# Performance work log

Hardware: AMD Instinct MI355X
Metric: run time of the kernel (lower is better)

Reference implementation:

```python
import jax, jax.numpy as jnp
import numpy as np

BN_EPS = 1e-5

def _bn(x, g, b, m, v):
    # eval-mode BatchNorm1d over channel dim of [B, C, N]
    scale = g / jnp.sqrt(v + BN_EPS)
    return (x - m[:, None]) * scale[:, None] + b[:, None]

def _conv1(W, x, b=None):
    # 1x1 Conv1d == channel matmul: W [O, C], x [B, C, N] -> [B, O, N]
    y = jnp.einsum('oc,bcn->bon', W, x)
    if b is not None:
        y = y + b[:, None]
    return y

def _sa_layer(x, wqk, wv, bv, wt, bt, g, b, m, v):
    # offset self-attention; q_conv and k_conv share weights
    xk = _conv1(wqk, x)                          # [B, D, N]
    xq = jnp.swapaxes(xk, 1, 2)                  # [B, N, D]
    xv = _conv1(wv, x, bv)                       # [B, D, N]
    energy = jnp.einsum('bnd,bdm->bnm', xq, xk)  # [B, N, N]
    attn = jax.nn.softmax(energy, axis=-1)
    attn = attn / (1e-9 + attn.sum(axis=1, keepdims=True))  # L1 renorm over dim=1
    x_r = jnp.einsum('bdn,bnm->bdm', xv, attn)   # [B, D, N]
    x_r = jax.nn.relu(_bn(_conv1(wt, x - x_r, bt), g, b, m, v))
    return x + x_r

def setup_inputs() -> dict:
    key = jax.random.key(0)
    ks = iter(jax.random.split(key, 64))
    B, Cin, N = 16, 3, 2048
    D, F, H1, OUT = 128, 1024, 512, 50
    def rn(shape, s=0.05):
        return jax.random.normal(next(ks), shape, dtype=jnp.float32) * s
    def var(shape):
        return jax.random.uniform(next(ks), shape, dtype=jnp.float32) * 0.5 + 0.5
    inp = {
        'x': jax.random.normal(next(ks), (B, Cin, N), dtype=jnp.float32),
        'w1': rn((D, Cin)), 'w2': rn((D, D)),
        'bn1_g': jnp.ones((D,)), 'bn1_b': jnp.zeros((D,)), 'bn1_m': rn((D,)), 'bn1_v': var((D,)),
        'bn2_g': jnp.ones((D,)), 'bn2_b': jnp.zeros((D,)), 'bn2_m': rn((D,)), 'bn2_v': var((D,)),
        'sa_wqk': rn((4, D, D)), 'sa_wv': rn((4, D, D)), 'sa_bv': rn((4, D)),
        'sa_wt': rn((4, D, D)), 'sa_bt': rn((4, D)),
        'sa_g': jnp.ones((4, D)), 'sa_b': jnp.zeros((4, D)), 'sa_m': rn((4, D)), 'sa_v': var((4, D)),
        'wf': rn((F, 4 * D)),
        'bnf_g': jnp.ones((F,)), 'bnf_b': jnp.zeros((F,)), 'bnf_m': rn((F,)), 'bnf_v': var((F,)),
        'ws1': rn((H1, 3 * F)), 'bs1': rn((H1,)),
        'bns1_g': jnp.ones((H1,)), 'bns1_b': jnp.zeros((H1,)), 'bns1_m': rn((H1,)), 'bns1_v': var((H1,)),
        'ws2': rn((OUT, H1)), 'bs2': rn((OUT,)),
        'bns2_g': jnp.ones((OUT,)), 'bns2_b': jnp.zeros((OUT,)), 'bns2_m': rn((OUT,)), 'bns2_v': var((OUT,)),
    }
    return inp

def reference(x, w1, w2, bn1_g, bn1_b, bn1_m, bn1_v, bn2_g, bn2_b, bn2_m, bn2_v,
              sa_wqk, sa_wv, sa_bv, sa_wt, sa_bt, sa_g, sa_b, sa_m, sa_v,
              wf, bnf_g, bnf_b, bnf_m, bnf_v,
              ws1, bs1, bns1_g, bns1_b, bns1_m, bns1_v,
              ws2, bs2, bns2_g, bns2_b, bns2_m, bns2_v):
    B, _, N = x.shape
    h = jax.nn.relu(_bn(_conv1(w1, x), bn1_g, bn1_b, bn1_m, bn1_v))
    h = jax.nn.relu(_bn(_conv1(w2, h), bn2_g, bn2_b, bn2_m, bn2_v))
    feats = []
    for i in range(4):
        h = _sa_layer(h, sa_wqk[i], sa_wv[i], sa_bv[i], sa_wt[i], sa_bt[i],
                      sa_g[i], sa_b[i], sa_m[i], sa_v[i])
        feats.append(h)
    cat = jnp.concatenate(feats, axis=1)                 # [B, 512, N]
    fused = _bn(_conv1(wf, cat), bnf_g, bnf_b, bnf_m, bnf_v)
    fused = jnp.where(fused >= 0, fused, 0.2 * fused)    # LeakyReLU(0.2)
    x_max = fused.max(axis=2)                            # [B, 1024]
    x_avg = fused.mean(axis=2)                           # [B, 1024]
    gmax = jnp.broadcast_to(x_max[:, :, None], (B, x_max.shape[1], N))
    gavg = jnp.broadcast_to(x_avg[:, :, None], (B, x_avg.shape[1], N))
    h = jnp.concatenate([fused, gmax, gavg], axis=1)     # [B, 3072, N]
    h = jax.nn.relu(_bn(_conv1(ws1, h, bs1), bns1_g, bns1_b, bns1_m, bns1_v))
    # dropout is identity in eval mode
    h = jax.nn.relu(_bn(_conv1(ws2, h, bs2), bns2_g, bns2_b, bns2_m, bns2_v))
    return h  # [B, out_channel, N]
```

## Files before the change

### kernel.cpp

```cpp
#include <hip/hip_runtime.h>
#include <cstdint>
#include <cstddef>

#define B_   16
#define N_   2048
#define D_   128
#define F_   1024
#define H1_  512
#define OUT_ 50

static constexpr float BN_EPS = 1e-5f;

typedef __attribute__((ext_vector_type(8))) short short8;
typedef __attribute__((ext_vector_type(4))) float f32x4;

__device__ inline unsigned short f2bf(float f) {
  union { float f; unsigned u; } v; v.f = f;
  unsigned r = v.u + 0x7fff + ((v.u >> 16) & 1);
  return (unsigned short)(r >> 16);
}
__device__ inline float bf2f(unsigned short h) {
  union { unsigned u; float f; } v; v.u = ((unsigned)h) << 16; return v.f;
}

__device__ inline void dma16(const unsigned short* g, unsigned short* l) {
  __builtin_amdgcn_global_load_lds(
      (const __attribute__((address_space(1))) unsigned int*)g,
      (__attribute__((address_space(3))) unsigned int*)l, 16, 0, 0);
}

__global__ void foldw_k(const float* __restrict__ W, int ldW,
                        const float* __restrict__ bias,
                        const float* __restrict__ g, const float* __restrict__ bb,
                        const float* __restrict__ m, const float* __restrict__ v,
                        unsigned short* __restrict__ Wb, float* __restrict__ biasF,
                        int O, int Opad, int K) {
  long i = (long)blockIdx.x * 256 + threadIdx.x;
  if (i >= (long)Opad * K) return;
  int o = (int)(i / K), k = (int)(i % K);
  float sc = 1.f, sh = 0.f;
  if (o < O && g) { sc = g[o] * rsqrtf(v[o] + BN_EPS); sh = bb[o] - m[o] * sc; }
  float w = (o < O) ? W[(long)o * ldW + k] * sc : 0.f;
  Wb[i] = f2bf(w);
  if (k == 0 && biasF) {
    float bf = 0.f;
    if (o < O) bf = (bias ? bias[o] : 0.f) * sc + sh;
    biasF[o] = bf;
  }
}

__global__ void conv1_k(const float* __restrict__ x, const float* __restrict__ w1,
                        const float* __restrict__ g, const float* __restrict__ bb,
                        const float* __restrict__ m, const float* __restrict__ v,
                        unsigned short* __restrict__ h0b) {
  int o = threadIdx.x, n = blockIdx.x, b = blockIdx.y;
  const float* xb = x + (long)b * 3 * N_;
  float val = w1[o * 3 + 0] * xb[n] + w1[o * 3 + 1] * xb[N_ + n] + w1[o * 3 + 2] * xb[2 * N_ + n];
  float sc = g[o] * rsqrtf(v[o] + BN_EPS);
  val = val * sc + (bb[o] - m[o] * sc);
  h0b[((long)b * N_ + n) * D_ + o] = f2bf(fmaxf(val, 0.f));
}

template <int TM>
__global__ __launch_bounds__(256, 4)
void gemm_tok(const unsigned short* __restrict__ Wb, int ldW,
              const unsigned short* __restrict__ A, long sA, int ldA,
              const float* __restrict__ biasF,
              const float* __restrict__ perBO, int ldPBO,
              const unsigned short* __restrict__ resH, long sRes, int ldRes,
              unsigned short* __restrict__ outH, long sOutH, int ldOutH,
              float* __restrict__ pmax, float* __restrict__ psum,
              int K, int act, int flags) {
  constexpr int MT = TM / 32;
  __shared__ unsigned short lAB[TM * 64 + 128 * 64];
  __shared__ float lpm[4][64], lps[4][64];
  unsigned short* lA = lAB;
  unsigned short* lB = lAB + TM * 64;
  unsigned short* lS = lAB;
  int tid = threadIdx.x;
  int n0 = blockIdx.x * TM, o0 = blockIdx.y * 128, b = blockIdx.z;
  int wave = tid >> 6, lane = tid & 63;
  int wr = wave >> 1, wc = wave & 1;
  int quad = lane >> 4, l15 = lane & 15;
  int rowL = lane >> 3;
  int kseg = (lane & 7) ^ rowL;
  const unsigned short* Ab = A + (long)b * sA + (long)n0 * ldA;
  const unsigned short* Wp = Wb + (long)o0 * ldW;

  f32x4 acc[MT][4];
  #pragma unroll
  for (int i = 0; i < MT; ++i)
    #pragma unroll
    for (int j = 0; j < 4; ++j) acc[i][j] = (f32x4){0.f, 0.f, 0.f, 0.f};

  for (int kc = 0; kc < K; kc += 64) {
    #pragma unroll
    for (int t = 0; t < 4; ++t) {
      int chunk = t * 4 + wave;
      dma16(Wp + (long)(chunk * 8 + rowL) * ldW + kc + kseg * 8, &lB[chunk * 512]);
      if (chunk < TM / 8)
        dma16(Ab + (long)(chunk * 8 + rowL) * ldA + kc + kseg * 8, &lA[chunk * 512]);
    }
    __syncthreads();
    #pragma unroll
    for (int kk = 0; kk < 2; ++kk) {
      short8 af[MT], bf[4];
      #pragma unroll
      for (int mt = 0; mt < MT; ++mt) {
        int r = wr * (TM / 2) + mt * 16 + l15;
        af[mt] = *(const short8*)&lA[r * 64 + (((kk * 4 + quad) ^ (l15 & 7)) * 8)];
      }
      #pragma unroll
      for (int ot = 0; ot < 4; ++ot) {
        int r = wc * 64 + ot * 16 + l15;
        bf[ot] = *(const short8*)&lB[r * 64 + (((kk * 4 + quad) ^ (l15 & 7)) * 8)];
      }
      #pragma unroll
      for (int mt = 0; mt < MT; ++mt)
        #pragma unroll
        for (int ot = 0; ot < 4; ++ot)
          acc[mt][ot] = __builtin_amdgcn_mfma_f32_16x16x32_bf16(bf[ot], af[mt], acc[mt][ot], 0, 0, 0);
    }
    __syncthreads();
  }

  bool doPool = (flags & 32) != 0;
  #pragma unroll
  for (int ot = 0; ot < 4; ++ot) {
    int obL = wc * 64 + ot * 16 + quad * 4;
    int ob = o0 + obL;
    float bi[4] = {0.f, 0.f, 0.f, 0.f};
    if (biasF) { float4 t = *(const float4*)&biasF[ob]; bi[0] = t.x; bi[1] = t.y; bi[2] = t.z; bi[3] = t.w; }
    if (perBO) {
      float4 t = *(const float4*)&perBO[(long)b * ldPBO + ob];
      bi[0] += t.x; bi[1] += t.y; bi[2] += t.z; bi[3] += t.w;
    }
    float pm4[4], ps4[4];
    #pragma unroll
    for (int r = 0; r < 4; ++r) { pm4[r] = -1e30f; ps4[r] = 0.f; }
    int g = obL >> 3, go = obL & 7;
    #pragma unroll
    for (int mt = 0; mt < MT; ++mt) {
      int nL = wr * (TM / 2) + mt * 16 + l15;
      float vals[4];
      #pragma unroll
      for (int r = 0; r < 4; ++r) {
        float val = acc[mt][ot][r] + bi[r];
        if (act == 1)      val = fmaxf(val, 0.f);
        else if (act == 2) val = (val >= 0.f) ? val : 0.2f * val;
        vals[r] = val;
      }
      if (flags & 16) {
        uint2 rv = *(const uint2*)&resH[(long)b * sRes + (long)(n0 + nL) * ldRes + ob];
        unsigned short rr[4];
        *(uint2*)rr = rv;
        #pragma unroll
        for (int r = 0; r < 4; ++r) vals[r] += bf2f(rr[r]);
      }
      unsigned short t4[4];
      #pragma unroll
      for (int r = 0; r < 4; ++r) {
        t4[r] = f2bf(vals[r]);
        if (doPool) { pm4[r] = fmaxf(pm4[r], vals[r]); ps4[r] += vals[r]; }
      }
      int gp = (g & 8) | ((g ^ (nL & 7)) & 7);
      *(uint2*)&lS[nL * 128 + gp * 8 + go] = *(uint2*)&t4[0];
    }
    if (doPool) {
      #pragma unroll
      for (int r = 0; r < 4; ++r) {
        float m = pm4[r], s = ps4[r];
        m = fmaxf(m, __shfl_xor(m, 1)); s += __shfl_xor(s, 1);
        m = fmaxf(m, __shfl_xor(m, 2)); s += __shfl_xor(s, 2);
        m = fmaxf(m, __shfl_xor(m, 4)); s += __shfl_xor(s, 4);
        m = fmaxf(m, __shfl_xor(m, 8)); s += __shfl_xor(s, 8);
        if (l15 == 0) { lpm[wave][ot * 16 + quad * 4 + r] = m; lps[wave][ot * 16 + quad * 4 + r] = s; }
      }
    }
  }
  __syncthreads();
  {
    int r0 = tid >> 4, s = tid & 15;
    #pragma unroll
    for (int it = 0; it < TM / 16; ++it) {
      int row = it * 16 + r0;
      int sp = (s & 8) | ((s ^ (row & 7)) & 7);
      short8 v = *(const short8*)&lS[row * 128 + sp * 8];
      *(short8*)&outH[(long)b * sOutH + (long)(n0 + row) * ldOutH + o0 + s * 8] = v;
    }
  }
  if (doPool && tid < 128) {
    int wcx = tid >> 6, ol = tid & 63;
    float m = fmaxf(lpm[wcx][ol], lpm[wcx + 2][ol]);
    float s = lps[wcx][ol] + lps[wcx + 2][ol];
    int o = o0 + wcx * 64 + ol;
    pmax[((long)b * 16 + blockIdx.x) * 1024 + o] = m;
    psum[((long)b * 16 + blockIdx.x) * 1024 + o] = s;
  }
}

template <int TM>
__global__ __launch_bounds__(256, 4)
void gemm_chan(const unsigned short* __restrict__ Wb, int ldW,
               const unsigned short* __restrict__ A, long sA, int ldA,
               const float* __restrict__ biasF,
               float* __restrict__ outF, long sOutF, int ldOutF,
               unsigned short* __restrict__ outH, long sOutH, int ldOutH,
               int K, int O, int act) {
  constexpr int MT = TM / 32;
  __shared__ unsigned short lA[TM * 64];
  __shared__ unsigned short lB[128 * 64];
  int tid = threadIdx.x;
  int n0 = blockIdx.x * TM, o0 = blockIdx.y * 128, b = blockIdx.z;
  int wave = tid >> 6, lane = tid & 63;
  int wr = wave >> 1, wc = wave & 1;
  int quad = lane >> 4, l15 = lane & 15;
  int rowL = lane >> 3;
  int kseg = (lane & 7) ^ rowL;
  const unsigned short* Ab = A + (long)b * sA + (long)n0 * ldA;
  const unsigned short* Wp = Wb + (long)o0 * ldW;

  f32x4 acc[MT][4];
  #pragma unroll
  for (int i = 0; i < MT; ++i)
    #pragma unroll
    for (int j = 0; j < 4; ++j) acc[i][j] = (f32x4){0.f, 0.f, 0.f, 0.f};

  for (int kc = 0; kc < K; kc += 64) {
    #pragma unroll
    for (int t = 0; t < 4; ++t) {
      int chunk = t * 4 + wave;
      dma16(Wp + (long)(chunk * 8 + rowL) * ldW + kc + kseg * 8, &lB[chunk * 512]);
      if (chunk < TM / 8)
        dma16(Ab + (long)(chunk * 8 + rowL) * ldA + kc + kseg * 8, &lA[chunk * 512]);
    }
    __syncthreads();
    #pragma unroll
    for (int kk = 0; kk < 2; ++kk) {
      short8 af[MT], bf[4];
      #pragma unroll
      for (int mt = 0; mt < MT; ++mt) {
        int r = wr * (TM / 2) + mt * 16 + l15;
        af[mt] = *(const short8*)&lA[r * 64 + (((kk * 4 + quad) ^ (l15 & 7)) * 8)];
      }
      #pragma unroll
      for (int ot = 0; ot < 4; ++ot) {
        int r = wc * 64 + ot * 16 + l15;
        bf[ot] = *(const short8*)&lB[r * 64 + (((kk * 4 + quad) ^ (l15 & 7)) * 8)];
      }
      #pragma unroll
      for (int mt = 0; mt < MT; ++mt)
        #pragma unroll
        for (int ot = 0; ot < 4; ++ot)
          acc[mt][ot] = __builtin_amdgcn_mfma_f32_16x16x32_bf16(af[mt], bf[ot], acc[mt][ot], 0, 0, 0);
    }
    __syncthreads();
  }

  #pragma unroll
  for (int ot = 0; ot < 4; ++ot) {
    int o = o0 + wc * 64 + ot * 16 + l15;
    if (o >= O) continue;
    float bi = biasF ? biasF[o] : 0.f;
    #pragma unroll
    for (int mt = 0; mt < MT; ++mt) {
      int nb = n0 + wr * (TM / 2) + mt * 16 + quad * 4;
      float vals[4];
      #pragma unroll
      for (int r = 0; r < 4; ++r) {
        float val = acc[mt][ot][r] + bi;
        if (act == 1)      val = fmaxf(val, 0.f);
        else if (act == 2) val = (val >= 0.f) ? val : 0.2f * val;
        vals[r] = val;
      }
      if (outF)
        *(float4*)&outF[(long)b * sOutF + (long)o * ldOutF + nb] = *(float4*)vals;
      if (outH) {
        unsigned short t[4];
        #pragma unroll
        for (int r = 0; r < 4; ++r) t[r] = f2bf(vals[r]);
        *(uint2*)&outH[(long)b * sOutH + (long)o * ldOutH + nb] = *(uint2*)&t[0];
      }
    }
  }
}

__global__ __launch_bounds__(256)
void gram_lw(const unsigned short* __restrict__ xk, long sXk,
             float* __restrict__ pm, float* __restrict__ ps) {
  __shared__ unsigned short lK[2][64 * 128];
  int tid = threadIdx.x, wave = tid >> 6, lane = tid & 63;
  int quad = lane >> 4, l15 = lane & 15;
  int rowL4 = lane >> 4, s16 = lane & 15;
  int n0 = blockIdx.y * 128, b = blockIdx.x, seg = blockIdx.z;
  int mbase = seg * 1024;
  const unsigned short* Kp = xk + (long)b * sXk;
  short8 afr[2][4];
  #pragma unroll
  for (int g2 = 0; g2 < 2; ++g2) {
    const unsigned short* arow = Kp + (long)(n0 + g2 * 64 + wave * 16 + l15) * 128;
    #pragma unroll
    for (int kf = 0; kf < 4; ++kf) afr[g2][kf] = *(const short8*)(arow + kf * 32 + quad * 8);
  }
  float runm[2][4], runs[2][4];
  #pragma unroll
  for (int g2 = 0; g2 < 2; ++g2)
    #pragma unroll
    for (int r = 0; r < 4; ++r) { runm[g2][r] = -1e30f; runs[g2][r] = 0.f; }

  auto stage = [&](int ch, int bf) {
    #pragma unroll
    for (int t = 0; t < 4; ++t) {
      int c = t * 4 + wave;
      int row = c * 4 + rowL4;
      int gseg = (s16 & 8) | ((s16 ^ (row & 7)) & 7);
      dma16(Kp + (long)(mbase + ch * 64 + row) * 128 + gseg * 8, &lK[bf][c * 512]);
    }
  };
  stage(0, 0);

  for (int ch = 0; ch < 16; ++ch) {
    __syncthreads();
    int bf = ch & 1;
    if (ch + 1 < 16) stage(ch + 1, bf ^ 1);
    f32x4 sv[2][4];
    #pragma unroll
    for (int mf = 0; mf < 4; ++mf) {
      f32x4 sa = (f32x4){0.f, 0.f, 0.f, 0.f};
      f32x4 sb = (f32x4){0.f, 0.f, 0.f, 0.f};
      #pragma unroll
      for (int kf = 0; kf < 4; ++kf) {
        int r = mf * 16 + l15, q = kf * 4 + quad;
        int sp = (q & 8) | ((q ^ (r & 7)) & 7);
        short8 bfr = *(const short8*)&lK[bf][r * 128 + sp * 8];
        sa = __builtin_amdgcn_mfma_f32_16x16x32_bf16(afr[0][kf], bfr, sa, 0, 0, 0);
        sb = __builtin_amdgcn_mfma_f32_16x16x32_bf16(afr[1][kf], bfr, sb, 0, 0, 0);
      }
      sv[0][mf] = sa; sv[1][mf] = sb;
    }
    #pragma unroll
    for (int g2 = 0; g2 < 2; ++g2)
      #pragma unroll
      for (int r = 0; r < 4; ++r) {
        float e0 = sv[g2][0][r], e1 = sv[g2][1][r], e2 = sv[g2][2][r], e3 = sv[g2][3][r];
        float cm = fmaxf(fmaxf(e0, e1), fmaxf(e2, e3));
        float mn = fmaxf(runm[g2][r], cm);
        runs[g2][r] = runs[g2][r] * __expf(runm[g2][r] - mn) +
                      (__expf(e0 - mn) + __expf(e1 - mn)) + (__expf(e2 - mn) + __expf(e3 - mn));
        runm[g2][r] = mn;
      }
  }
  #pragma unroll
  for (int g2 = 0; g2 < 2; ++g2)
    #pragma unroll
    for (int r = 0; r < 4; ++r) {
      float m = runm[g2][r], s = runs[g2][r];
      #pragma unroll
      for (int off = 1; off < 16; off <<= 1) {
        float mo = __shfl_xor(m, off), so = __shfl_xor(s, off);
        float mn = fmaxf(m, mo);
        s = s * __expf(m - mn) + so * __expf(mo - mn);
        m = mn;
      }
      if (l15 == 0) {
        int n = n0 + g2 * 64 + wave * 16 + quad * 4 + r;
        pm[((long)b * 2 + seg) * 2048 + n] = m;
        ps[((long)b * 2 + seg) * 2048 + n] = s;
      }
    }
}

__global__ void lwred_k(const float* __restrict__ pm, const float* __restrict__ ps,
                        float* __restrict__ lw) {
  int n = blockIdx.x * 256 + threadIdx.x, b = blockIdx.y;
  float m0 = pm[((long)b * 2) * 2048 + n], m1 = pm[((long)b * 2 + 1) * 2048 + n];
  float s0 = ps[((long)b * 2) * 2048 + n], s1 = ps[((long)b * 2 + 1) * 2048 + n];
  float mx = fmaxf(m0, m1);
  float s = s0 * __expf(m0 - mx) + s1 * __expf(m1 - mx);
  lw[(long)b * 2048 + n] = mx + __logf(s);
}

__global__ __launch_bounds__(256)
void pv_k(const unsigned short* __restrict__ xk, long sXk,
          const unsigned short* __restrict__ xv, long sXv,
          const float* __restrict__ lw,
          float* __restrict__ pacc, float* __restrict__ pc) {
  __shared__ unsigned short lK[64 * 128];
  __shared__ unsigned short lV[128 * 64];
  __shared__ float lwt[64];
  int tid = threadIdx.x, wave = tid >> 6, lane = tid & 63;
  int quad = lane >> 4, l15 = lane & 15;
  int rowL4 = lane >> 4, s16 = lane & 15;
  int rowL8 = lane >> 3, s8 = lane & 7;
  int m0 = blockIdx.y * 128, b = blockIdx.x, seg = blockIdx.z;
  int nbase = seg * 1024;
  const unsigned short* Kp = xk + (long)b * sXk;
  const unsigned short* Vp = xv + (long)b * sXv;
  short8 akr[2][4];
  #pragma unroll
  for (int g2 = 0; g2 < 2; ++g2) {
    const unsigned short* arow = Kp + (long)(m0 + g2 * 64 + wave * 16 + l15) * 128;
    #pragma unroll
    for (int kf = 0; kf < 4; ++kf) akr[g2][kf] = *(const short8*)(arow + kf * 32 + quad * 8);
  }
  f32x4 acc[2][8];
  #pragma unroll
  for (int g2 = 0; g2 < 2; ++g2)
    #pragma unroll
    for (int dt = 0; dt < 8; ++dt) acc[g2][dt] = (f32x4){0.f, 0.f, 0.f, 0.f};
  float runc[2] = {0.f, 0.f};

  for (int ch = 0; ch < 16; ++ch) {
    if (ch) __syncthreads();
    #pragma unroll
    for (int t = 0; t < 4; ++t) {
      int c = t * 4 + wave;
      int rowK = c * 4 + rowL4;
      int gsegK = (s16 & 8) | ((s16 ^ (rowK & 7)) & 7);
      dma16(Kp + (long)(nbase + ch * 64 + rowK) * 128 + gsegK * 8, &lK[c * 512]);
      int rowV = c * 8 + rowL8;
      int gsegV = s8 ^ (rowV & 7);
      dma16(Vp + (long)rowV * 2048 + nbase + ch * 64 + gsegV * 8, &lV[c * 512]);
    }
    if (tid < 64) lwt[tid] = lw[(long)b * 2048 + nbase + ch * 64 + tid];
    __syncthreads();
    unsigned pd0[2][4], pd1[2][4];
    #pragma unroll
    for (int nf = 0; nf < 4; ++nf) {
      f32x4 sa = (f32x4){0.f, 0.f, 0.f, 0.f};
      f32x4 sb = (f32x4){0.f, 0.f, 0.f, 0.f};
      #pragma unroll
      for (int kf = 0; kf < 4; ++kf) {
        int r = nf * 16 + l15, q = kf * 4 + quad;
        int sp = (q & 8) | ((q ^ (r & 7)) & 7);
        short8 kfr = *(const short8*)&lK[r * 128 + sp * 8];
        sa = __builtin_amdgcn_mfma_f32_16x16x32_bf16(kfr, akr[0][kf], sa, 0, 0, 0);
        sb = __builtin_amdgcn_mfma_f32_16x16x32_bf16(kfr, akr[1][kf], sb, 0, 0, 0);
      }
      float4 lw4 = *(const float4*)&lwt[nf * 16 + quad * 4];
      float lwv[4] = {lw4.x, lw4.y, lw4.z, lw4.w};
      unsigned short ta[4], tb[4];
      #pragma unroll
      for (int r = 0; r < 4; ++r) {
        float p0 = __expf(sa[r] - lwv[r]);
        float p1 = __expf(sb[r] - lwv[r]);
        runc[0] += p0; runc[1] += p1;
        ta[r] = f2bf(p0); tb[r] = f2bf(p1);
      }
      pd0[0][nf] = (unsigned)ta[0] | ((unsigned)ta[1] << 16);
      pd1[0][nf] = (unsigned)ta[2] | ((unsigned)ta[3] << 16);
      pd0[1][nf] = (unsigned)tb[0] | ((unsigned)tb[1] << 16);
      pd1[1][nf] = (unsigned)tb[2] | ((unsigned)tb[3] << 16);
    }
    #pragma unroll
    for (int kc = 0; kc < 2; ++kc) {
      short8 paf[2];
      #pragma unroll
      for (int g2 = 0; g2 < 2; ++g2) {
        unsigned d0 = (quad >= 2) ? pd0[g2][2 * kc + 1] : pd0[g2][2 * kc];
        unsigned d1 = (quad >= 2) ? pd1[g2][2 * kc + 1] : pd1[g2][2 * kc];
        int s0 = ((quad & 1) << 5) + l15;
        union { unsigned u[4]; short8 v; } pu;
        pu.u[0] = (unsigned)__shfl((int)d0, s0);
        pu.u[1] = (unsigned)__shfl((int)d1, s0);
        pu.u[2] = (unsigned)__shfl((int)d0, s0 + 16);
        pu.u[3] = (unsigned)__shfl((int)d1, s0 + 16);
        paf[g2] = pu.v;
      }
      #pragma unroll
      for (int dt = 0; dt < 8; ++dt) {
        int r = dt * 16 + l15;
        int spv = (kc * 4 + quad) ^ (r & 7);
        short8 vb = *(const short8*)&lV[r * 64 + spv * 8];
        acc[0][dt] = __builtin_amdgcn_mfma_f32_16x16x32_bf16(paf[0], vb, acc[0][dt], 0, 0, 0);
        acc[1][dt] = __builtin_amdgcn_mfma_f32_16x16x32_bf16(paf[1], vb, acc[1][dt], 0, 0, 0);
      }
    }
  }
  #pragma unroll
  for (int g2 = 0; g2 < 2; ++g2) {
    float s = runc[g2];
    s += __shfl_xor(s, 16);
    s += __shfl_xor(s, 32);
    if (quad == 0)
      pc[((long)b * 2 + seg) * 2048 + m0 + g2 * 64 + wave * 16 + l15] = s;
  }
  float* pa = pacc + ((long)b * 2 + seg) * 262144;
  #pragma unroll
  for (int g2 = 0; g2 < 2; ++g2)
    #pragma unroll
    for (int dt = 0; dt < 8; ++dt) {
      int d = dt * 16 + l15;
      #pragma unroll
      for (int r = 0; r < 4; ++r)
        pa[(long)(m0 + g2 * 64 + wave * 16 + quad * 4 + r) * 128 + d] = acc[g2][dt][r];
    }
}

__global__ __launch_bounds__(256)
void pvred_k(const float* __restrict__ pacc, const float* __restrict__ pc,
             const unsigned short* __restrict__ lib, long sLi, int ldLi,
             unsigned short* __restrict__ xrb, long sXr) {
  int i = blockIdx.x * 256 + threadIdx.x;
  int b = blockIdx.y;
  int m = i >> 5, d4 = (i & 31) * 4;
  float4 a0 = *(const float4*)&pacc[((long)b * 2 + 0) * 262144 + (long)m * 128 + d4];
  float4 a1 = *(const float4*)&pacc[((long)b * 2 + 1) * 262144 + (long)m * 128 + d4];
  float c = pc[((long)b * 2) * 2048 + m] + pc[((long)b * 2 + 1) * 2048 + m];
  float inv = 1.f / (1e-9f + c);
  uint2 lv = *(const uint2*)&lib[(long)b * sLi + (long)m * ldLi + d4];
  unsigned short lr[4];
  *(uint2*)lr = lv;
  unsigned short o[4];
  o[0] = f2bf(bf2f(lr[0]) - (a0.x + a1.x) * inv);
  o[1] = f2bf(bf2f(lr[1]) - (a0.y + a1.y) * inv);
  o[2] = f2bf(bf2f(lr[2]) - (a0.z + a1.z) * inv);
  o[3] = f2bf(bf2f(lr[3]) - (a0.w + a1.w) * inv);
  *(uint2*)&xrb[(long)b * sXr + (long)m * 128 + d4] = *(uint2*)&o[0];
}

__global__ void poolred_k(const float* __restrict__ pmax, const float* __restrict__ psum,
                          float* __restrict__ xmax, float* __restrict__ xavg) {
  int f = blockIdx.x * 256 + threadIdx.x, b = blockIdx.y;
  float mx = -1e30f, s = 0.f;
  #pragma unroll
  for (int t = 0; t < 16; ++t) {
    mx = fmaxf(mx, pmax[((long)b * 16 + t) * 1024 + f]);
    s += psum[((long)b * 16 + t) * 1024 + f];
  }
  xmax[(long)b * 1024 + f] = mx;
  xavg[(long)b * 1024 + f] = s * (1.f / 2048.f);
}

__global__ __launch_bounds__(256)
void poolterm_k(const float* __restrict__ ws1, const float* __restrict__ xmax,
                const float* __restrict__ xavg,
                const float* __restrict__ bg, const float* __restrict__ bv,
                float* __restrict__ pt) {
  int o = blockIdx.x, b = blockIdx.y, tid = threadIdx.x;
  const float* w = ws1 + (long)o * 3072;
  float s = 0.f;
  #pragma unroll
  for (int it = 0; it < 4; ++it) {
    int c = tid + it * 256;
    s += w[1024 + c] * xmax[(long)b * 1024 + c] + w[2048 + c] * xavg[(long)b * 1024 + c];
  }
  #pragma unroll
  for (int off = 32; off; off >>= 1) s += __shfl_xor(s, off);
  __shared__ float rsm[4];
  if ((tid & 63) == 0) rsm[tid >> 6] = s;
  __syncthreads();
  if (tid == 0) {
    float sc = bg[o] * rsqrtf(bv[o] + BN_EPS);
    pt[(long)b * H1_ + o] = sc * (rsm[0] + rsm[1] + rsm[2] + rsm[3]);
  }
}

extern "C" void kernel_launch(void* const* d_in, const int* in_sizes, int n_in,
                              void* d_out, int out_size, void* d_ws, size_t ws_size,
                              hipStream_t stream) {
  const float* x      = (const float*)d_in[0];
  const float* w1     = (const float*)d_in[1];
  const float* w2     = (const float*)d_in[2];
  const float* bn1_g  = (const float*)d_in[3];
  const float* bn1_b  = (const float*)d_in[4];
  const float* bn1_m  = (const float*)d_in[5];
  const float* bn1_v  = (const float*)d_in[6];
  const float* bn2_g  = (const float*)d_in[7];
  const float* bn2_b  = (const float*)d_in[8];
  const float* bn2_m  = (const float*)d_in[9];
  const float* bn2_v  = (const float*)d_in[10];
  const float* sa_wqk = (const float*)d_in[11];
  const float* sa_wv  = (const float*)d_in[12];
  const float* sa_bv  = (const float*)d_in[13];
  const float* sa_wt  = (const float*)d_in[14];
  const float* sa_bt  = (const float*)d_in[15];
  const float* sa_g   = (const float*)d_in[16];
  const float* sa_b   = (const float*)d_in[17];
  const float* sa_m   = (const float*)d_in[18];
  const float* sa_v   = (const float*)d_in[19];
  const float* wf     = (const float*)d_in[20];
  const float* bnf_g  = (const float*)d_in[21];
  const float* bnf_b  = (const float*)d_in[22];
  const float* bnf_m  = (const float*)d_in[23];
  const float* bnf_v  = (const float*)d_in[24];
  const float* ws1    = (const float*)d_in[25];
  const float* bs1    = (const float*)d_in[26];
  const float* bns1_g = (const float*)d_in[27];
  const float* bns1_b = (const float*)d_in[28];
  const float* bns1_m = (const float*)d_in[29];
  const float* bns1_v = (const float*)d_in[30];
  const float* ws2    = (const float*)d_in[31];
  const float* bs2    = (const float*)d_in[32];
  const float* bns2_g = (const float*)d_in[33];
  const float* bns2_b = (const float*)d_in[34];
  const float* bns2_m = (const float*)d_in[35];
  const float* bns2_v = (const float*)d_in[36];
  float* out = (float*)d_out;

  float* ws = (float*)d_ws;
  size_t off = 0;
  auto alloc  = [&](size_t n) { float* p = ws + off; off += (n + 63) & ~(size_t)63; return p; };
  auto allocH = [&](size_t n) { return (unsigned short*)alloc((n + 1) / 2); };

  unsigned short* w2b  = allocH(128 * 128);
  unsigned short* wqkb = allocH(4 * 128 * 128);
  unsigned short* wvb  = allocH(4 * 128 * 128);
  unsigned short* wtb  = allocH(4 * 128 * 128);
  unsigned short* wfb  = allocH((size_t)F_ * 512);
  unsigned short* ws1b = allocH((size_t)H1_ * 1024);
  unsigned short* ws2b = allocH((size_t)128 * 512);
  float* bias_w2 = alloc(128);
  float* bias_v  = alloc(512);
  float* bias_t  = alloc(512);
  float* bias_f  = alloc(1024);
  float* bias_s1 = alloc(512);
  float* bias_s2 = alloc(128);
  float* lwB  = alloc((size_t)16 * 2048);
  float* pmax = alloc((size_t)16 * 16 * 1024);
  float* psum = alloc((size_t)16 * 16 * 1024);
  float* xmaxB = alloc((size_t)16 * 1024);
  float* xavgB = alloc((size_t)16 * 1024);
  float* ptB   = alloc((size_t)16 * 512);
  size_t fixedOff = off;

  const size_t perB = 131072 + 524288 + 1048576 + 131072 + 131072 + 131072 +
                      524288 + 12288;
  size_t wsFloats = ws_size / 4;
  int Gb = 1;
  for (int c : {16, 8, 4, 2, 1}) {
    if (fixedOff + (size_t)c * perB + 4096 <= wsFloats) { Gb = c; break; }
  }

  unsigned short* h1b    = allocH((size_t)Gb * 262144);
  unsigned short* featsb = allocH((size_t)Gb * 1048576);
  unsigned short* fusedb = allocH((size_t)Gb * 2097152);
  unsigned short* xkb    = allocH((size_t)Gb * 262144);
  unsigned short* xvb    = allocH((size_t)Gb * 262144);
  unsigned short* xrb    = allocH((size_t)Gb * 262144);
  float* paccB = alloc((size_t)Gb * 2 * 262144);
  float* pmB   = alloc((size_t)Gb * 2 * 2048);
  float* psB   = alloc((size_t)Gb * 2 * 2048);
  float* pcB   = alloc((size_t)Gb * 2 * 2048);
  unsigned short* h0b  = xrb;
  unsigned short* hs1b = featsb;

  foldw_k<<<64, 256, 0, stream>>>(w2, 128, nullptr, bn2_g, bn2_b, bn2_m, bn2_v,
                                  w2b, bias_w2, 128, 128, 128);
  for (int i = 0; i < 4; ++i) {
    foldw_k<<<64, 256, 0, stream>>>(sa_wqk + (size_t)i * 16384, 128, nullptr,
                                    nullptr, nullptr, nullptr, nullptr,
                                    wqkb + (size_t)i * 16384, nullptr, 128, 128, 128);
    foldw_k<<<64, 256, 0, stream>>>(sa_wv + (size_t)i * 16384, 128, sa_bv + i * 128,
                                    nullptr, nullptr, nullptr, nullptr,
                                    wvb + (size_t)i * 16384, bias_v + i * 128, 128, 128, 128);
    foldw_k<<<64, 256, 0, stream>>>(sa_wt + (size_t)i * 16384, 128, sa_bt + i * 128,
                                    sa_g + i * 128, sa_b + i * 128, sa_m + i * 128, sa_v + i * 128,
                                    wtb + (size_t)i * 16384, bias_t + i * 128, 128, 128, 128);
  }
  foldw_k<<<2048, 256, 0, stream>>>(wf, 512, nullptr, bnf_g, bnf_b, bnf_m, bnf_v,
                                    wfb, bias_f, 1024, 1024, 512);
  foldw_k<<<2048, 256, 0, stream>>>(ws1, 3072, bs1, bns1_g, bns1_b, bns1_m, bns1_v,
                                    ws1b, bias_s1, 512, 512, 1024);
  foldw_k<<<256, 256, 0, stream>>>(ws2, 512, bs2, bns2_g, bns2_b, bns2_m, bns2_v,
                                   ws2b, bias_s2, 50, 128, 512);

  const long sAct = 262144, sFeat = 1048576, sFus = 2097152;
  for (int b0 = 0; b0 < B_; b0 += Gb) {
    int g = Gb;
    conv1_k<<<dim3(N_, g), 128, 0, stream>>>(x + (long)b0 * 3 * N_, w1,
                                             bn1_g, bn1_b, bn1_m, bn1_v, h0b);
    gemm_tok<64><<<dim3(32, 1, g), 256, 0, stream>>>(
        w2b, 128, h0b, sAct, 128, bias_w2, nullptr, 0, nullptr, 0, 0,
        h1b, sAct, 128, nullptr, nullptr, 128, 1, 0);

    for (int i = 0; i < 4; ++i) {
      const unsigned short* lib = (i == 0) ? h1b : featsb + (size_t)(i - 1) * 128;
      int ldLi = (i == 0) ? 128 : 512;
      long sLi = (i == 0) ? sAct : sFeat;
      gemm_tok<64><<<dim3(32, 1, g), 256, 0, stream>>>(
          wqkb + (size_t)i * 16384, 128, lib, sLi, ldLi, nullptr, nullptr, 0,
          nullptr, 0, 0, xkb, sAct, 128, nullptr, nullptr, 128, 0, 0);
      gemm_chan<64><<<dim3(32, 1, g), 256, 0, stream>>>(
          wvb + (size_t)i * 16384, 128, lib, sLi, ldLi, bias_v + i * 128,
          nullptr, 0, 0, xvb, sAct, 2048, 128, 128, 0);
      gram_lw<<<dim3(g, 16, 2), 256, 0, stream>>>(xkb, sAct, pmB, psB);
      lwred_k<<<dim3(8, g), 256, 0, stream>>>(pmB, psB, lwB);
      pv_k<<<dim3(g, 16, 2), 256, 0, stream>>>(xkb, sAct, xvb, sAct, lwB, paccB, pcB);
      pvred_k<<<dim3(256, g), 256, 0, stream>>>(paccB, pcB, lib, sLi, ldLi, xrb, sAct);
      gemm_tok<64><<<dim3(32, 1, g), 256, 0, stream>>>(
          wtb + (size_t)i * 16384, 128, xrb, sAct, 128, bias_t + i * 128, nullptr, 0,
          lib, sLi, ldLi,
          featsb + (size_t)i * 128, sFeat, 512, nullptr, nullptr, 128, 1, 16);
    }

    gemm_tok<128><<<dim3(16, 8, g), 256, 0, stream>>>(
        wfb, 512, featsb, sFeat, 512, bias_f, nullptr, 0, nullptr, 0, 0,
        fusedb, sFus, 1024, pmax, psum, 512, 2, 32);
    poolred_k<<<dim3(4, g), 256, 0, stream>>>(pmax, psum, xmaxB, xavgB);
    poolterm_k<<<dim3(512, g), 256, 0, stream>>>(ws1, xmaxB, xavgB, bns1_g, bns1_v, ptB);
    gemm_tok<128><<<dim3(16, 4, g), 256, 0, stream>>>(
        ws1b, 1024, fusedb, sFus, 1024, bias_s1, ptB, 512, nullptr, 0, 0,
        hs1b, sFeat, 512, nullptr, nullptr, 1024, 1, 0);
    gemm_chan<64><<<dim3(32, 1, g), 256, 0, stream>>>(
        ws2b, 512, hs1b, sFeat, 512, bias_s2,
        out + (long)b0 * OUT_ * N_, (long)OUT_ * N_, 2048, nullptr, 0, 0,
        512, 50, 1);
  }
}
```

Before: 761.4 us.

## Fuse K/V projections, fold log-sum reduction into PV, shrink small GEMM tiles

The separate xk and xv projection kernels become one gemm_kv kernel. It picks the weight matrix and output layout from blockIdx.y, so both projections share one launch. The lwred_k kernel is removed, and pv_k now combines the two softmax partial max/sum segments itself when it loads each chunk. Several 128-wide GEMMs switch from 64-token to 32-token tiles, doubling block count for better occupancy. The aim is fewer launches and more parallelism on small GEMMs, at the cost of recomputing the log-sum-exp per PV block and possibly lower MFMA efficiency per block.

```diff
diff --git a/kernel.cpp b/kernel.cpp
--- a/kernel.cpp
+++ b/kernel.cpp
@@ -71,7 +71,7 @@
               unsigned short* __restrict__ outH, long sOutH, int ldOutH,
               float* __restrict__ pmax, float* __restrict__ psum,
               int K, int act, int flags) {
-  constexpr int MT = TM / 32;
+  constexpr int MT = (TM + 31) / 32;
   __shared__ unsigned short lAB[TM * 64 + 128 * 64];
   __shared__ float lpm[4][64], lps[4][64];
   unsigned short* lA = lAB;
@@ -207,7 +207,7 @@
                float* __restrict__ outF, long sOutF, int ldOutF,
                unsigned short* __restrict__ outH, long sOutH, int ldOutH,
                int K, int O, int act) {
-  constexpr int MT = TM / 32;
+  constexpr int MT = (TM + 31) / 32;
   __shared__ unsigned short lA[TM * 64];
   __shared__ unsigned short lB[128 * 64];
   int tid = threadIdx.x;
@@ -285,6 +285,112 @@
   }
 }
 
+__global__ __launch_bounds__(256, 4)
+void gemm_kv(const unsigned short* __restrict__ Wqk, const unsigned short* __restrict__ Wv,
+             const float* __restrict__ biasV,
+             const unsigned short* __restrict__ A, long sA, int ldA,
+             unsigned short* __restrict__ xk, long sXk,
+             unsigned short* __restrict__ xv, long sXv) {
+  __shared__ unsigned short lAB[64 * 64 + 128 * 64];
+  unsigned short* lA = lAB;
+  unsigned short* lB = lAB + 64 * 64;
+  unsigned short* lS = lAB;
+  int tid = threadIdx.x;
+  int n0 = blockIdx.x * 64, path = blockIdx.y, b = blockIdx.z;
+  int wave = tid >> 6, lane = tid & 63;
+  int wr = wave >> 1, wc = wave & 1;
+  int quad = lane >> 4, l15 = lane & 15;
+  int rowL = lane >> 3;
+  int kseg = (lane & 7) ^ rowL;
+  const unsigned short* Ab = A + (long)b * sA + (long)n0 * ldA;
+  const unsigned short* Wp = path ? Wv : Wqk;
+
+  f32x4 acc[2][4];
+  #pragma unroll
+  for (int i = 0; i < 2; ++i)
+    #pragma unroll
+    for (int j = 0; j < 4; ++j) acc[i][j] = (f32x4){0.f, 0.f, 0.f, 0.f};
+
+  for (int kc = 0; kc < 128; kc += 64) {
+    #pragma unroll
+    for (int t = 0; t < 4; ++t) {
+      int chunk = t * 4 + wave;
+      dma16(Wp + (long)(chunk * 8 + rowL) * 128 + kc + kseg * 8, &lB[chunk * 512]);
+      if (chunk < 8)
+        dma16(Ab + (long)(chunk * 8 + rowL) * ldA + kc + kseg * 8, &lA[chunk * 512]);
+    }
+    __syncthreads();
+    #pragma unroll
+    for (int kk = 0; kk < 2; ++kk) {
+      short8 af[2], bf[4];
+      #pragma unroll
+      for (int mt = 0; mt < 2; ++mt) {
+        int r = wr * 32 + mt * 16 + l15;
+        af[mt] = *(const short8*)&lA[r * 64 + (((kk * 4 + quad) ^ (l15 & 7)) * 8)];
+      }
+      #pragma unroll
+      for (int ot = 0; ot < 4; ++ot) {
+        int r = wc * 64 + ot * 16 + l15;
+        bf[ot] = *(const short8*)&lB[r * 64 + (((kk * 4 + quad) ^ (l15 & 7)) * 8)];
+      }
+      if (path == 0) {
+        #pragma unroll
+        for (int mt = 0; mt < 2; ++mt)
+          #pragma unroll
+          for (int ot = 0; ot < 4; ++ot)
+            acc[mt][ot] = __builtin_amdgcn_mfma_f32_16x16x32_bf16(bf[ot], af[mt], acc[mt][ot], 0, 0, 0);
+      } else {
+        #pragma unroll
+        for (int mt = 0; mt < 2; ++mt)
+          #pragma unroll
+          for (int ot = 0; ot < 4; ++ot)
+            acc[mt][ot] = __builtin_amdgcn_mfma_f32_16x16x32_bf16(af[mt], bf[ot], acc[mt][ot], 0, 0, 0);
+      }
+    }
+    __syncthreads();
+  }
+
+  if (path == 0) {
+    #pragma unroll
+    for (int ot = 0; ot < 4; ++ot) {
+      int obL = wc * 64 + ot * 16 + quad * 4;
+      int g = obL >> 3, go = obL & 7;
+      #pragma unroll
+      for (int mt = 0; mt < 2; ++mt) {
+        int nL = wr * 32 + mt * 16 + l15;
+        unsigned short t4[4];
+        #pragma unroll
+        for (int r = 0; r < 4; ++r) t4[r] = f2bf(acc[mt][ot][r]);
+        int gp = (g & 8) | ((g ^ (nL & 7)) & 7);
+        *(uint2*)&lS[nL * 128 + gp * 8 + go] = *(uint2*)&t4[0];
+      }
+    }
+    __syncthreads();
+    int r0 = tid >> 4, s = tid & 15;
+    #pragma unroll
+    for (int it = 0; it < 4; ++it) {
+      int row = it * 16 + r0;
+      int sp = (s & 8) | ((s ^ (row & 7)) & 7);
+      short8 v = *(const short8*)&lS[row * 128 + sp * 8];
+      *(short8*)&xk[(long)b * sXk + (long)(n0 + row) * 128 + s * 8] = v;
+    }
+  } else {
+    #pragma unroll
+    for (int ot = 0; ot < 4; ++ot) {
+      int o = wc * 64 + ot * 16 + l15;
+      float bi = biasV[o];
+      #pragma unroll
+      for (int mt = 0; mt < 2; ++mt) {
+        int nb = n0 + wr * 32 + mt * 16 + quad * 4;
+        unsigned short t[4];
+        #pragma unroll
+        for (int r = 0; r < 4; ++r) t[r] = f2bf(acc[mt][ot][r] + bi);
+        *(uint2*)&xv[(long)b * sXv + (long)o * 2048 + nb] = *(uint2*)&t[0];
+      }
+    }
+  }
+}
+
 __global__ __launch_bounds__(256)
 void gram_lw(const unsigned short* __restrict__ xk, long sXk,
              float* __restrict__ pm, float* __restrict__ ps) {
@@ -370,20 +476,10 @@
     }
 }
 
-__global__ void lwred_k(const float* __restrict__ pm, const float* __restrict__ ps,
-                        float* __restrict__ lw) {
-  int n = blockIdx.x * 256 + threadIdx.x, b = blockIdx.y;
-  float m0 = pm[((long)b * 2) * 2048 + n], m1 = pm[((long)b * 2 + 1) * 2048 + n];
-  float s0 = ps[((long)b * 2) * 2048 + n], s1 = ps[((long)b * 2 + 1) * 2048 + n];
-  float mx = fmaxf(m0, m1);
-  float s = s0 * __expf(m0 - mx) + s1 * __expf(m1 - mx);
-  lw[(long)b * 2048 + n] = mx + __logf(s);
-}
-
 __global__ __launch_bounds__(256)
 void pv_k(const unsigned short* __restrict__ xk, long sXk,
           const unsigned short* __restrict__ xv, long sXv,
-          const float* __restrict__ lw,
+          const float* __restrict__ pm, const float* __restrict__ ps,
           float* __restrict__ pacc, float* __restrict__ pc) {
   __shared__ unsigned short lK[64 * 128];
   __shared__ unsigned short lV[128 * 64];
@@ -422,7 +518,13 @@
       int gsegV = s8 ^ (rowV & 7);
       dma16(Vp + (long)rowV * 2048 + nbase + ch * 64 + gsegV * 8, &lV[c * 512]);
     }
-    if (tid < 64) lwt[tid] = lw[(long)b * 2048 + nbase + ch * 64 + tid];
+    if (tid < 64) {
+      int n = nbase + ch * 64 + tid;
+      float m0v = pm[((long)b * 2) * 2048 + n], m1v = pm[((long)b * 2 + 1) * 2048 + n];
+      float s0v = ps[((long)b * 2) * 2048 + n], s1v = ps[((long)b * 2 + 1) * 2048 + n];
+      float mx = fmaxf(m0v, m1v);
+      lwt[tid] = mx + __logf(s0v * __expf(m0v - mx) + s1v * __expf(m1v - mx));
+    }
     __syncthreads();
     unsigned pd0[2][4], pd1[2][4];
     #pragma unroll
@@ -616,7 +718,6 @@
   float* bias_f  = alloc(1024);
   float* bias_s1 = alloc(512);
   float* bias_s2 = alloc(128);
-  float* lwB  = alloc((size_t)16 * 2048);
   float* pmax = alloc((size_t)16 * 16 * 1024);
   float* psum = alloc((size_t)16 * 16 * 1024);
   float* xmaxB = alloc((size_t)16 * 1024);
@@ -670,7 +771,7 @@
     int g = Gb;
     conv1_k<<<dim3(N_, g), 128, 0, stream>>>(x + (long)b0 * 3 * N_, w1,
                                              bn1_g, bn1_b, bn1_m, bn1_v, h0b);
-    gemm_tok<64><<<dim3(32, 1, g), 256, 0, stream>>>(
+    gemm_tok<32><<<dim3(64, 1, g), 256, 0, stream>>>(
         w2b, 128, h0b, sAct, 128, bias_w2, nullptr, 0, nullptr, 0, 0,
         h1b, sAct, 128, nullptr, nullptr, 128, 1, 0);
 
@@ -678,17 +779,13 @@
       const unsigned short* lib = (i == 0) ? h1b : featsb + (size_t)(i - 1) * 128;
       int ldLi = (i == 0) ? 128 : 512;
       long sLi = (i == 0) ? sAct : sFeat;
-      gemm_tok<64><<<dim3(32, 1, g), 256, 0, stream>>>(
-          wqkb + (size_t)i * 16384, 128, lib, sLi, ldLi, nullptr, nullptr, 0,
-          nullptr, 0, 0, xkb, sAct, 128, nullptr, nullptr, 128, 0, 0);
-      gemm_chan<64><<<dim3(32, 1, g), 256, 0, stream>>>(
-          wvb + (size_t)i * 16384, 128, lib, sLi, ldLi, bias_v + i * 128,
-          nullptr, 0, 0, xvb, sAct, 2048, 128, 128, 0);
+      gemm_kv<<<dim3(32, 2, g), 256, 0, stream>>>(
+          wqkb + (size_t)i * 16384, wvb + (size_t)i * 16384, bias_v + i * 128,
+          lib, sLi, ldLi, xkb, sAct, xvb, sAct);
       gram_lw<<<dim3(g, 16, 2), 256, 0, stream>>>(xkb, sAct, pmB, psB);
-      lwred_k<<<dim3(8, g), 256, 0, stream>>>(pmB, psB, lwB);
-      pv_k<<<dim3(g, 16, 2), 256, 0, stream>>>(xkb, sAct, xvb, sAct, lwB, paccB, pcB);
+      pv_k<<<dim3(g, 16, 2), 256, 0, stream>>>(xkb, sAct, xvb, sAct, pmB, psB, paccB, pcB);
       pvred_k<<<dim3(256, g), 256, 0, stream>>>(paccB, pcB, lib, sLi, ldLi, xrb, sAct);
-      gemm_tok<64><<<dim3(32, 1, g), 256, 0, stream>>>(
+      gemm_tok<32><<<dim3(64, 1, g), 256, 0, stream>>>(
           wtb + (size_t)i * 16384, 128, xrb, sAct, 128, bias_t + i * 128, nullptr, 0,
           lib, sLi, ldLi,
           featsb + (size_t)i * 128, sFeat, 512, nullptr, nullptr, 128, 1, 16);
@@ -702,7 +799,7 @@
     gemm_tok<128><<<dim3(16, 4, g), 256, 0, stream>>>(
         ws1b, 1024, fusedb, sFus, 1024, bias_s1, ptB, 512, nullptr, 0, 0,
         hs1b, sFeat, 512, nullptr, nullptr, 1024, 1, 0);
-    gemm_chan<64><<<dim3(32, 1, g), 256, 0, stream>>>(
+    gemm_chan<32><<<dim3(64, 1, g), 256, 0, stream>>>(
         ws2b, 512, hs1b, sFeat, 512, bias_s2,
         out + (long)b0 * OUT_ * N_, (long)OUT_ * N_, 2048, nullptr, 0, 0,
         512, 50, 1);
```

Measured after the change: 703.0 us. 7.7% less time.
